# Optimization experiments

Measured on AMD Instinct MI355X. Metric: run time of the kernel, lower is better.

Reference implementation:

```python
import jax, jax.numpy as jnp
import numpy as np

B, T, D = 32, 576, 1024          # T = (384//16)**2 patches
H, G, HD = 16, 4, 64             # num_heads, query_groups, head_dim
BASE = 10000.0
SCALE = 1.0 / float(np.sqrt(HD))


def _rope2d(x):
    # x: [B, T, nH, HD]; 2D rotary: split head_dim into 4 groups of freq_dim.
    b, t, nh, hd = x.shape
    fd = hd // 4
    grid = int(np.sqrt(t))
    inv_freq = 1.0 / (BASE ** (jnp.arange(fd, dtype=jnp.float32) / fd))  # [fd]
    pos = jnp.arange(grid, dtype=jnp.float32)
    gx, gy = jnp.meshgrid(pos, pos, indexing='ij')          # [grid, grid]
    theta_x = gx.reshape(-1)[:, None] * inv_freq            # [T, fd]
    theta_y = gy.reshape(-1)[:, None] * inv_freq            # [T, fd]
    sx = jnp.sin(theta_x)[None, :, None, :]                 # [1, T, 1, fd]
    cx = jnp.cos(theta_x)[None, :, None, :]
    sy = jnp.sin(theta_y)[None, :, None, :]
    cy = jnp.cos(theta_y)[None, :, None, :]
    xr = x.reshape(b, t, nh, 4, fd)
    x1, x2, y1, y2 = xr[..., 0, :], xr[..., 1, :], xr[..., 2, :], xr[..., 3, :]
    out = jnp.stack([x1 * cx - x2 * sx,
                     x1 * sx + x2 * cx,
                     y1 * cy - y2 * sy,
                     y1 * sy + y2 * cy], axis=-2)           # [B, T, nH, 4, fd]
    return out.reshape(b, t, nh, hd)


def setup_inputs() -> dict:
    key = jax.random.key(0)
    k1, k2, k3 = jax.random.split(key, 3)
    x = jax.random.normal(k1, (B, T, D), dtype=jnp.float32)
    w_qkv = jax.random.normal(k2, (H * HD + 2 * G * HD, D), dtype=jnp.float32) * 0.02
    w_o = jax.random.normal(k3, (D, H * HD), dtype=jnp.float32) * 0.02
    return {"x": x, "w_qkv": w_qkv, "w_o": w_o, "window_size": -1}


def reference(x, w_qkv, w_o, window_size):
    # window_size=-1 -> full (non-windowed) attention, matching SDPA fallback.
    b, t, _ = x.shape
    qkv = x @ w_qkv.T                                       # [B, T, H*HD + 2*G*HD]
    q, k, v = jnp.split(qkv, [H * HD, H * HD + G * HD], axis=-1)
    q = q.reshape(b, t, H, HD)
    k = k.reshape(b, t, G, HD)
    v = v.reshape(b, t, G, HD)
    q = _rope2d(q)
    k = _rope2d(k)
    q = q.transpose(0, 2, 1, 3)                             # [B, H, T, HD]
    k = k.transpose(0, 2, 1, 3)                             # [B, G, T, HD]
    v = v.transpose(0, 2, 1, 3)
    hpg = H // G
    k = jnp.repeat(k, hpg, axis=1)                          # [B, H, T, HD]
    v = jnp.repeat(v, hpg, axis=1)
    scores = jnp.einsum('bhqd,bhkd->bhqk', q, k) * SCALE    # [B, H, T, T]
    attn = jax.nn.softmax(scores, axis=-1)
    out = jnp.einsum('bhqk,bhkd->bhqd', attn, v)            # [B, H, T, HD]
    out = out.transpose(0, 2, 1, 3).reshape(b, t, H * HD)
    return out @ w_o.T                                      # [B, T, D]
```

## Files before the change

kernel.cpp:

```cpp
#include <hip/hip_runtime.h>

typedef unsigned short u16;
typedef unsigned long long u64;
typedef __attribute__((ext_vector_type(8))) short short8;
typedef __attribute__((ext_vector_type(4))) float f32x4;

#define B_ 32
#define T_ 576
#define H_ 16
#define G_ 4
#define HD_ 64
#define DM 1024
#define NQKV 1536
#define BT (B_*T_)
#define GRID2D 24
#define FD 16

__device__ __forceinline__ u16 f2bf(float f) {
  unsigned u = __float_as_uint(f);
  u = (u + 0x7FFFu + ((u >> 16) & 1u)) >> 16;
  return (u16)u;
}
__device__ __forceinline__ float exp2v(float x) {
  float r;
  asm("v_exp_f32 %0, %1" : "=v"(r) : "v"(x));
  return r;
}

__device__ __forceinline__ void gl_lds16(const u16* g, u16* lds) {
  __builtin_amdgcn_global_load_lds((const __attribute__((address_space(1))) unsigned int*)g,
                                   (__attribute__((address_space(3))) unsigned int*)lds, 16, 0, 0);
}

__global__ __launch_bounds__(256) void cvt_kernel(const float4* __restrict__ in, u16* __restrict__ o, int n4) {
  int i = blockIdx.x * 256 + threadIdx.x;
  if (i >= n4) return;
  float4 v = in[i];
  u64 pk = (u64)f2bf(v.x) | ((u64)f2bf(v.y) << 16) | ((u64)f2bf(v.z) << 32) | ((u64)f2bf(v.w) << 48);
  *(u64*)(o + (size_t)i * 4) = pk;
}

__global__ __launch_bounds__(256) void rope_table_kernel(float4* __restrict__ tab) {
  int i = blockIdx.x * 256 + threadIdx.x;
  if (i >= T_ * FD) return;
  int t = i >> 4, j = i & 15;
  float inv = powf(10000.0f, -(float)j / 16.0f);
  float tx = (float)(t / GRID2D) * inv;
  float ty = (float)(t % GRID2D) * inv;
  float4 r;
  r.x = sinf(tx); r.y = cosf(tx); r.z = sinf(ty); r.w = cosf(ty);
  tab[i] = r;
}

__device__ __forceinline__ void stage_ab(const u16* __restrict__ A, const u16* __restrict__ Bw,
                                         int m0, int n0, int k0, u16* Asb, u16* Bsb,
                                         int w, int srow, int skk) {
#pragma unroll
  for (int ii = 0; ii < 2; ++ii) {
    int i = w * 2 + ii;
    int row = i * 16 + srow;
    gl_lds16(A + (size_t)(m0 + row) * DM + k0 + skk, Asb + i * 512);
    gl_lds16(Bw + (size_t)(n0 + row) * DM + k0 + skk, Bsb + i * 512);
  }
}

#define WAITBAR(N)                                        \
  __builtin_amdgcn_sched_barrier(0);                      \
  asm volatile("s_waitcnt vmcnt(" #N ")\n\ts_barrier" ::: "memory"); \
  __builtin_amdgcn_sched_barrier(0);

template <int EPI, int NX>
__global__ __launch_bounds__(256) void gemm_nt(const u16* __restrict__ A, const u16* __restrict__ Bw,
                                               u16* __restrict__ o0, u16* __restrict__ o1,
                                               u16* __restrict__ o2, float* __restrict__ fo,
                                               const float4* __restrict__ tab) {
  __shared__ __align__(16) u16 As[3][128 * 32];
  __shared__ __align__(16) u16 Bs[3][128 * 32];
  const int tid = threadIdx.x;
  const int w = tid >> 6, l = tid & 63;
  const int wm = w >> 1, wn = w & 1;
  const int L = blockIdx.y * NX + blockIdx.x;
  const int cpx = (NX * 144) / 8;
  const int W = (L & 7) * cpx + (L >> 3);
  const int by = W / NX, bx = W - by * NX;
  const int m0 = by * 128, n0 = bx * 128;
  const int lr = l & 15, lg = l >> 4;
  const int srow = l >> 2;
  const int skk = (l & 3) * 8;
  f32x4 acc[4][4] = {};

#define COMPUTE(buf)                                                                        \
  {                                                                                         \
    short8 af[4], bfr[4];                                                                   \
    _Pragma("unroll") for (int mi = 0; mi < 4; ++mi)                                        \
        af[mi] = *(const short8*)(&As[buf][(wm * 64 + mi * 16 + lr) * 32 + lg * 8]);        \
    _Pragma("unroll") for (int ni = 0; ni < 4; ++ni)                                        \
        bfr[ni] = *(const short8*)(&Bs[buf][(wn * 64 + ni * 16 + lr) * 32 + lg * 8]);       \
    __builtin_amdgcn_s_setprio(1);                                                          \
    _Pragma("unroll") for (int mi = 0; mi < 4; ++mi)                                        \
        _Pragma("unroll") for (int ni = 0; ni < 4; ++ni)                                    \
            acc[mi][ni] = __builtin_amdgcn_mfma_f32_16x16x32_bf16(af[mi], bfr[ni],          \
                                                                  acc[mi][ni], 0, 0, 0);    \
    __builtin_amdgcn_s_setprio(0);                                                          \
  }

  stage_ab(A, Bw, m0, n0, 0,  &As[0][0], &Bs[0][0], w, srow, skk);
  stage_ab(A, Bw, m0, n0, 32, &As[1][0], &Bs[1][0], w, srow, skk);
  WAITBAR(4)

  int ic = 0;
  for (int t = 0; t < 30; ++t) {
    int in2 = ic + 2; if (in2 >= 3) in2 -= 3;
    stage_ab(A, Bw, m0, n0, (t + 2) * 32, &As[in2][0], &Bs[in2][0], w, srow, skk);
    COMPUTE(ic);
    WAITBAR(4)
    ++ic; if (ic == 3) ic = 0;
  }
  COMPUTE(0);
  WAITBAR(0)
  COMPUTE(1);
#undef COMPUTE

  if (EPI == 0) {
    const float qs = 0.125f * 1.44269504f;
    const int nbase = n0 + wn * 64;
#pragma unroll
    for (int mi = 0; mi < 4; ++mi) {
#pragma unroll
      for (int r = 0; r < 4; ++r) {
        int mg = m0 + wm * 64 + mi * 16 + lg * 4 + r;
        int bb = mg / T_, t = mg - bb * T_;
        float v0 = acc[mi][0][r], v1 = acc[mi][1][r], v2 = acc[mi][2][r], v3 = acc[mi][3][r];
        if (nbase < 1280) {
          float4 tb = tab[t * FD + lr];
          float sc = (nbase < 1024) ? qs : 1.0f;
          float e0 = (v0 * tb.y - v1 * tb.x) * sc;
          float e1 = (v0 * tb.x + v1 * tb.y) * sc;
          float e2 = (v2 * tb.w - v3 * tb.z) * sc;
          float e3 = (v2 * tb.z + v3 * tb.w) * sc;
          u16* dst;
          if (nbase < 1024) {
            int h = nbase >> 6;
            dst = o0 + (((size_t)bb * H_ + h) * T_ + t) * 64 + lr;
          } else {
            int g = (nbase - 1024) >> 6;
            dst = o1 + (((size_t)bb * G_ + g) * T_ + t) * 64 + lr;
          }
          dst[0] = f2bf(e0); dst[16] = f2bf(e1); dst[32] = f2bf(e2); dst[48] = f2bf(e3);
        } else {
          int g = (nbase - 1280) >> 6;
          u16* dst = o2 + ((size_t)bb * G_ + g) * (64 * (size_t)T_) + t;
          dst[(0 * 16 + lr) * (size_t)T_] = f2bf(v0);
          dst[(1 * 16 + lr) * (size_t)T_] = f2bf(v1);
          dst[(2 * 16 + lr) * (size_t)T_] = f2bf(v2);
          dst[(3 * 16 + lr) * (size_t)T_] = f2bf(v3);
        }
      }
    }
  } else {
#pragma unroll
    for (int mi = 0; mi < 4; ++mi)
#pragma unroll
      for (int ni = 0; ni < 4; ++ni)
#pragma unroll
        for (int r = 0; r < 4; ++r) {
          int mg = m0 + wm * 64 + mi * 16 + lg * 4 + r;
          int ng = n0 + wn * 64 + ni * 16 + lr;
          fo[(size_t)mg * 1024 + ng] = acc[mi][ni][r];
        }
  }
}

__device__ __forceinline__ void stage_kv(const u16* __restrict__ k, const u16* __restrict__ vt,
                                         size_t kvbase, int kt, u16* Ksb, u16* Vsb,
                                         int w, int srow, int sblk) {
#pragma unroll
  for (int ii = 0; ii < 2; ++ii) {
    int i = w * 2 + ii;
    int row = i * 8 + srow;
    gl_lds16(k + kvbase + (size_t)(kt * 64 + row) * 64 + sblk * 8, Ksb + i * 512);
    gl_lds16(vt + kvbase + (size_t)row * T_ + kt * 64 + sblk * 8, Vsb + i * 512);
  }
}

__global__ __launch_bounds__(256) void attn_kernel(const u16* __restrict__ q, const u16* __restrict__ k,
                                                   const u16* __restrict__ vt, u16* __restrict__ o) {
  __shared__ __align__(16) u16 Ks[2][64 * 64];
  __shared__ __align__(16) u16 Vs[2][64 * 64];
  __shared__ __align__(16) u16 Pl[4][16 * 72];
  int L = blockIdx.x;
  int W = (L & 7) * 576 + (L >> 3);
  int qt = W % 9;
  int bh = W / 9;
  int h = bh & 15, b = bh >> 4;
  int g = h >> 2;
  int tid = threadIdx.x;
  int w = tid >> 6, l = tid & 63;
  int lr = l & 15, lg = l >> 4;
  const size_t kvbase = ((size_t)(b * G_ + g)) * (T_ * 64);

  const u16* qptr = q + (((size_t)(b * H_ + h)) * T_ + qt * 64 + w * 16 + lr) * 64;
  short8 qf0 = *(const short8*)(qptr + lg * 8);
  short8 qf1 = *(const short8*)(qptr + 32 + lg * 8);

  float ls[4] = {0.f, 0.f, 0.f, 0.f};
  f32x4 oacc[4];
#pragma unroll
  for (int dt = 0; dt < 4; ++dt) oacc[dt] = (f32x4){0.f, 0.f, 0.f, 0.f};

  const int srow = l >> 3;
  const int sblk = (l & 7) ^ (srow & 7);

  stage_kv(k, vt, kvbase, 0, &Ks[0][0], &Vs[0][0], w, srow, sblk);
  asm volatile("s_waitcnt vmcnt(0)\n\ts_barrier" ::: "memory");

  int cur = 0;
  for (int kt = 0; kt < 9; ++kt) {
    if (kt < 8)
      stage_kv(k, vt, kvbase, kt + 1, &Ks[cur ^ 1][0], &Vs[cur ^ 1][0], w, srow, sblk);

    f32x4 sacc[4];
#pragma unroll
    for (int ct = 0; ct < 4; ++ct) {
      sacc[ct] = (f32x4){0.f, 0.f, 0.f, 0.f};
      int row = ct * 16 + lr;
      int i0 = (0 * 4 + lg) ^ (row & 7);
      int i1 = (1 * 4 + lg) ^ (row & 7);
      short8 kf0 = *(const short8*)(&Ks[cur][row * 64 + i0 * 8]);
      short8 kf1 = *(const short8*)(&Ks[cur][row * 64 + i1 * 8]);
      sacc[ct] = __builtin_amdgcn_mfma_f32_16x16x32_bf16(qf0, kf0, sacc[ct], 0, 0, 0);
      sacc[ct] = __builtin_amdgcn_mfma_f32_16x16x32_bf16(qf1, kf1, sacc[ct], 0, 0, 0);
    }

    float p[4][4];
#pragma unroll
    for (int ct = 0; ct < 4; ++ct)
#pragma unroll
      for (int r = 0; r < 4; ++r) p[ct][r] = exp2v(sacc[ct][r]);
#pragma unroll
    for (int r = 0; r < 4; ++r) ls[r] += (p[0][r] + p[1][r]) + (p[2][r] + p[3][r]);

    u16* pl = &Pl[w][0];
#pragma unroll
    for (int ct = 0; ct < 4; ++ct)
#pragma unroll
      for (int r = 0; r < 4; ++r)
        pl[(lg * 4 + r) * 72 + ct * 16 + lr] = (u16)((__float_as_uint(p[ct][r]) + 0x8000u) >> 16);
    asm volatile("s_waitcnt lgkmcnt(0)" ::: "memory");
#pragma unroll
    for (int c = 0; c < 2; ++c) {
      short8 pf = *(const short8*)(pl + lr * 72 + c * 32 + lg * 8);
#pragma unroll
      for (int dt = 0; dt < 4; ++dt) {
        int row = dt * 16 + lr;
        int blk = (c * 4 + lg) ^ (row & 7);
        short8 vf = *(const short8*)(&Vs[cur][row * 64 + blk * 8]);
        oacc[dt] = __builtin_amdgcn_mfma_f32_16x16x32_bf16(pf, vf, oacc[dt], 0, 0, 0);
      }
    }

    if (kt < 8) {
      asm volatile("s_waitcnt vmcnt(0)\n\ts_barrier" ::: "memory");
      cur ^= 1;
    }
  }

#pragma unroll
  for (int mk = 1; mk <= 8; mk <<= 1)
#pragma unroll
    for (int r = 0; r < 4; ++r) ls[r] += __shfl_xor(ls[r], mk);

#pragma unroll
  for (int dt = 0; dt < 4; ++dt)
#pragma unroll
    for (int r = 0; r < 4; ++r) {
      int trow = qt * 64 + w * 16 + lg * 4 + r;
      float v = oacc[dt][r] / ls[r];
      o[((size_t)b * T_ + trow) * 1024 + h * 64 + dt * 16 + lr] = f2bf(v);
    }
}

extern "C" void kernel_launch(void* const* d_in, const int* in_sizes, int n_in,
                              void* d_out, int out_size, void* d_ws, size_t ws_size,
                              hipStream_t stream) {
  const float* x = (const float*)d_in[0];
  const float* wqkv = (const float*)d_in[1];
  const float* wo = (const float*)d_in[2];
  float* out = (float*)d_out;

  u16* ws = (u16*)d_ws;
  u16* xb = ws;
  u16* wqkvb = xb + (size_t)BT * DM;
  u16* wob = wqkvb + (size_t)NQKV * DM;
  u16* qb = wob + (size_t)DM * DM;
  u16* kb = qb + (size_t)BT * DM;
  u16* vtb = kb + (size_t)B_ * G_ * T_ * 64;
  float4* tab = (float4*)(vtb + (size_t)B_ * G_ * T_ * 64);
  u16* ob = xb;

  cvt_kernel<<<(BT * DM / 4 + 255) / 256, 256, 0, stream>>>((const float4*)x, xb, BT * DM / 4);
  cvt_kernel<<<(NQKV * DM / 4 + 255) / 256, 256, 0, stream>>>((const float4*)wqkv, wqkvb, NQKV * DM / 4);
  cvt_kernel<<<(DM * DM / 4 + 255) / 256, 256, 0, stream>>>((const float4*)wo, wob, DM * DM / 4);
  rope_table_kernel<<<(T_ * FD + 255) / 256, 256, 0, stream>>>(tab);
  gemm_nt<0, 12><<<dim3(12, 144), 256, 0, stream>>>(xb, wqkvb, qb, kb, vtb, nullptr, tab);
  attn_kernel<<<B_ * H_ * 9, 256, 0, stream>>>(qb, kb, vtb, ob);
  gemm_nt<1, 8><<<dim3(8, 144), 256, 0, stream>>>(ob, wob, nullptr, nullptr, nullptr, out, nullptr);
}
```

Measured before the change: 285.6 us.

## Use 256x256 tile GEMM with 512 threads for QKV projection

```diff
diff --git a/kernel.cpp b/kernel.cpp
--- a/kernel.cpp
+++ b/kernel.cpp
@@ -32,6 +32,11 @@
                                    (__attribute__((address_space(3))) unsigned int*)lds, 16, 0, 0);
 }
 
+#define WAITBAR(N)                                        \
+  __builtin_amdgcn_sched_barrier(0);                      \
+  asm volatile("s_waitcnt vmcnt(" #N ")\n\ts_barrier" ::: "memory"); \
+  __builtin_amdgcn_sched_barrier(0);
+
 __global__ __launch_bounds__(256) void cvt_kernel(const float4* __restrict__ in, u16* __restrict__ o, int n4) {
   int i = blockIdx.x * 256 + threadIdx.x;
   if (i >= n4) return;
@@ -52,6 +57,104 @@
   tab[i] = r;
 }
 
+__global__ __launch_bounds__(512, 1) void gemm256_qkv(const u16* __restrict__ A, const u16* __restrict__ Bw,
+                                                      u16* __restrict__ o0, u16* __restrict__ o1,
+                                                      u16* __restrict__ o2,
+                                                      const float4* __restrict__ tab) {
+  __shared__ __align__(16) u16 As[3][256 * 32];
+  __shared__ __align__(16) u16 Bs[3][256 * 32];
+  const int tid = threadIdx.x;
+  const int w = tid >> 6, l = tid & 63;
+  const int wm = w >> 2, wn = w & 3;
+  const int L = blockIdx.y * 6 + blockIdx.x;
+  const int W = (L & 7) * 54 + (L >> 3);
+  const int by = W / 6, bx = W - by * 6;
+  const int m0 = by * 256, n0 = bx * 256;
+  const int lr = l & 15, lg = l >> 4;
+  const int srow = tid >> 2;
+  const int skk = (tid & 3) * 8;
+
+  f32x4 acc[8][4] = {};
+
+#define STAGE(buf, kt)                                                                     \
+  {                                                                                        \
+    const int k0_ = (kt) * 32;                                                             \
+    gl_lds16(A + (size_t)(m0 + srow) * DM + k0_ + skk,        &As[buf][(size_t)tid * 8]);  \
+    gl_lds16(A + (size_t)(m0 + 128 + srow) * DM + k0_ + skk,  &As[buf][4096 + (size_t)tid * 8]); \
+    gl_lds16(Bw + (size_t)(n0 + srow) * DM + k0_ + skk,       &Bs[buf][(size_t)tid * 8]);  \
+    gl_lds16(Bw + (size_t)(n0 + 128 + srow) * DM + k0_ + skk, &Bs[buf][4096 + (size_t)tid * 8]); \
+  }
+
+#define COMPUTE(buf)                                                                        \
+  {                                                                                         \
+    short8 af[8], bfr[4];                                                                   \
+    _Pragma("unroll") for (int mi = 0; mi < 8; ++mi)                                        \
+        af[mi] = *(const short8*)(&As[buf][(wm * 128 + mi * 16 + lr) * 32 + lg * 8]);       \
+    _Pragma("unroll") for (int ni = 0; ni < 4; ++ni)                                        \
+        bfr[ni] = *(const short8*)(&Bs[buf][(wn * 64 + ni * 16 + lr) * 32 + lg * 8]);       \
+    __builtin_amdgcn_s_setprio(1);                                                          \
+    _Pragma("unroll") for (int mi = 0; mi < 8; ++mi)                                        \
+        _Pragma("unroll") for (int ni = 0; ni < 4; ++ni)                                    \
+            acc[mi][ni] = __builtin_amdgcn_mfma_f32_16x16x32_bf16(af[mi], bfr[ni],          \
+                                                                  acc[mi][ni], 0, 0, 0);    \
+    __builtin_amdgcn_s_setprio(0);                                                          \
+  }
+
+  STAGE(0, 0)
+  STAGE(1, 1)
+  WAITBAR(4)
+
+  int ic = 0;
+  for (int t = 0; t < 30; ++t) {
+    int in2 = ic + 2; if (in2 >= 3) in2 -= 3;
+    STAGE(in2, t + 2)
+    COMPUTE(ic);
+    WAITBAR(4)
+    ++ic; if (ic == 3) ic = 0;
+  }
+  COMPUTE(0);
+  WAITBAR(0)
+  COMPUTE(1);
+#undef COMPUTE
+#undef STAGE
+
+  const float qs = 0.125f * 1.44269504f;
+  const int nbase = n0 + wn * 64;
+#pragma unroll
+  for (int mi = 0; mi < 8; ++mi) {
+#pragma unroll
+    for (int r = 0; r < 4; ++r) {
+      int mg = m0 + wm * 128 + mi * 16 + lg * 4 + r;
+      int bb = mg / T_, t = mg - bb * T_;
+      float v0 = acc[mi][0][r], v1 = acc[mi][1][r], v2 = acc[mi][2][r], v3 = acc[mi][3][r];
+      if (nbase < 1280) {
+        float4 tb = tab[t * FD + lr];
+        float sc = (nbase < 1024) ? qs : 1.0f;
+        float e0 = (v0 * tb.y - v1 * tb.x) * sc;
+        float e1 = (v0 * tb.x + v1 * tb.y) * sc;
+        float e2 = (v2 * tb.w - v3 * tb.z) * sc;
+        float e3 = (v2 * tb.z + v3 * tb.w) * sc;
+        u16* dst;
+        if (nbase < 1024) {
+          int h = nbase >> 6;
+          dst = o0 + (((size_t)bb * H_ + h) * T_ + t) * 64 + lr;
+        } else {
+          int g = (nbase - 1024) >> 6;
+          dst = o1 + (((size_t)bb * G_ + g) * T_ + t) * 64 + lr;
+        }
+        dst[0] = f2bf(e0); dst[16] = f2bf(e1); dst[32] = f2bf(e2); dst[48] = f2bf(e3);
+      } else {
+        int g = (nbase - 1280) >> 6;
+        u16* dst = o2 + ((size_t)bb * G_ + g) * (64 * (size_t)T_) + t;
+        dst[(0 * 16 + lr) * (size_t)T_] = f2bf(v0);
+        dst[(1 * 16 + lr) * (size_t)T_] = f2bf(v1);
+        dst[(2 * 16 + lr) * (size_t)T_] = f2bf(v2);
+        dst[(3 * 16 + lr) * (size_t)T_] = f2bf(v3);
+      }
+    }
+  }
+}
+
 __device__ __forceinline__ void stage_ab(const u16* __restrict__ A, const u16* __restrict__ Bw,
                                          int m0, int n0, int k0, u16* Asb, u16* Bsb,
                                          int w, int srow, int skk) {
@@ -64,16 +167,9 @@
   }
 }
 
-#define WAITBAR(N)                                        \
-  __builtin_amdgcn_sched_barrier(0);                      \
-  asm volatile("s_waitcnt vmcnt(" #N ")\n\ts_barrier" ::: "memory"); \
-  __builtin_amdgcn_sched_barrier(0);
-
-template <int EPI, int NX>
+template <int NX>
 __global__ __launch_bounds__(256) void gemm_nt(const u16* __restrict__ A, const u16* __restrict__ Bw,
-                                               u16* __restrict__ o0, u16* __restrict__ o1,
-                                               u16* __restrict__ o2, float* __restrict__ fo,
-                                               const float4* __restrict__ tab) {
+                                               float* __restrict__ fo) {
   __shared__ __align__(16) u16 As[3][128 * 32];
   __shared__ __align__(16) u16 Bs[3][128 * 32];
   const int tid = threadIdx.x;
@@ -121,54 +217,16 @@
   COMPUTE(1);
 #undef COMPUTE
 
-  if (EPI == 0) {
-    const float qs = 0.125f * 1.44269504f;
-    const int nbase = n0 + wn * 64;
-#pragma unroll
-    for (int mi = 0; mi < 4; ++mi) {
+#pragma unroll
+  for (int mi = 0; mi < 4; ++mi)
+#pragma unroll
+    for (int ni = 0; ni < 4; ++ni)
 #pragma unroll
       for (int r = 0; r < 4; ++r) {
         int mg = m0 + wm * 64 + mi * 16 + lg * 4 + r;
-        int bb = mg / T_, t = mg - bb * T_;
-        float v0 = acc[mi][0][r], v1 = acc[mi][1][r], v2 = acc[mi][2][r], v3 = acc[mi][3][r];
-        if (nbase < 1280) {
-          float4 tb = tab[t * FD + lr];
-          float sc = (nbase < 1024) ? qs : 1.0f;
-          float e0 = (v0 * tb.y - v1 * tb.x) * sc;
-          float e1 = (v0 * tb.x + v1 * tb.y) * sc;
-          float e2 = (v2 * tb.w - v3 * tb.z) * sc;
-          float e3 = (v2 * tb.z + v3 * tb.w) * sc;
-          u16* dst;
-          if (nbase < 1024) {
-            int h = nbase >> 6;
-            dst = o0 + (((size_t)bb * H_ + h) * T_ + t) * 64 + lr;
-          } else {
-            int g = (nbase - 1024) >> 6;
-            dst = o1 + (((size_t)bb * G_ + g) * T_ + t) * 64 + lr;
-          }
-          dst[0] = f2bf(e0); dst[16] = f2bf(e1); dst[32] = f2bf(e2); dst[48] = f2bf(e3);
-        } else {
-          int g = (nbase - 1280) >> 6;
-          u16* dst = o2 + ((size_t)bb * G_ + g) * (64 * (size_t)T_) + t;
-          dst[(0 * 16 + lr) * (size_t)T_] = f2bf(v0);
-          dst[(1 * 16 + lr) * (size_t)T_] = f2bf(v1);
-          dst[(2 * 16 + lr) * (size_t)T_] = f2bf(v2);
-          dst[(3 * 16 + lr) * (size_t)T_] = f2bf(v3);
-        }
+        int ng = n0 + wn * 64 + ni * 16 + lr;
+        fo[(size_t)mg * 1024 + ng] = acc[mi][ni][r];
       }
-    }
-  } else {
-#pragma unroll
-    for (int mi = 0; mi < 4; ++mi)
-#pragma unroll
-      for (int ni = 0; ni < 4; ++ni)
-#pragma unroll
-        for (int r = 0; r < 4; ++r) {
-          int mg = m0 + wm * 64 + mi * 16 + lg * 4 + r;
-          int ng = n0 + wn * 64 + ni * 16 + lr;
-          fo[(size_t)mg * 1024 + ng] = acc[mi][ni][r];
-        }
-  }
 }
 
 __device__ __forceinline__ void stage_kv(const u16* __restrict__ k, const u16* __restrict__ vt,
@@ -302,7 +360,7 @@
   cvt_kernel<<<(NQKV * DM / 4 + 255) / 256, 256, 0, stream>>>((const float4*)wqkv, wqkvb, NQKV * DM / 4);
   cvt_kernel<<<(DM * DM / 4 + 255) / 256, 256, 0, stream>>>((const float4*)wo, wob, DM * DM / 4);
   rope_table_kernel<<<(T_ * FD + 255) / 256, 256, 0, stream>>>(tab);
-  gemm_nt<0, 12><<<dim3(12, 144), 256, 0, stream>>>(xb, wqkvb, qb, kb, vtb, nullptr, tab);
+  gemm256_qkv<<<dim3(6, 72), 512, 0, stream>>>(xb, wqkvb, qb, kb, vtb, tab);
   attn_kernel<<<B_ * H_ * 9, 256, 0, stream>>>(qb, kb, vtb, ob);
-  gemm_nt<1, 8><<<dim3(8, 144), 256, 0, stream>>>(ob, wob, nullptr, nullptr, nullptr, out, nullptr);
-}
+  gemm_nt<8><<<dim3(8, 144), 256, 0, stream>>>(ob, wob, out);
+}
```

After: 309.1 us. 1.08x slower.
